# Optimization experiments

Measured on AMD Instinct MI355X. Metric: run time of the kernel, lower is better.

The kernel has to match this reference:

```python
import jax, jax.numpy as jnp
import numpy as np

B, N, IN, OUT, H = 8, 1024, 256, 256, 4
D = OUT // H  # head_dim = 64


def setup_inputs() -> dict:
    key = jax.random.key(0)
    k1, k2, k3, k4 = jax.random.split(key, 4)
    h = jax.random.normal(k1, (B, N, IN), dtype=jnp.float32)
    # torch Linear weight: [out, in], Wh = h @ W.T
    W = jax.random.normal(k2, (H * D, IN), dtype=jnp.float32) * (1.0 / np.sqrt(IN))
    # attention vector a: [n_heads, 2*head_dim] (xavier-uniform-ish scale)
    a = jax.random.normal(k3, (H, 2 * D), dtype=jnp.float32) * 0.1
    adj_mask = jax.random.bernoulli(k4, 0.1, (B, N, N))
    # ensure every row has at least one neighbor (self-loop) to avoid all -inf rows
    adj_mask = adj_mask | jnp.eye(N, dtype=bool)[None]
    return {"h": h, "W": W, "a": a, "adj_mask": adj_mask}


def reference(h, W, a, adj_mask):
    # Wh: [B, H, N, D]
    Wh = (h @ W.T).reshape(B, N, H, D).transpose(0, 2, 1, 3)
    # Split 'a' into src/dst halves: e_ij = leaky_relu(a_src.Wh_i + a_dst.Wh_j)
    # (mathematically identical to the original concat+einsum, without the N^2*2D tensor)
    src = jnp.einsum('bhnd,hd->bhn', Wh, a[:, :D])
    dst = jnp.einsum('bhnd,hd->bhn', Wh, a[:, D:])
    e = jax.nn.leaky_relu(src[:, :, :, None] + dst[:, :, None, :], negative_slope=0.2)
    e = jnp.where(adj_mask[:, None, :, :], e, -jnp.inf)
    att = jax.nn.softmax(e, axis=-1)
    att = jnp.where(jnp.isnan(att), 0.0, att)
    # dropout in eval mode -> identity
    h_prime = jnp.einsum('bhij,bhjd->bhid', att, Wh)
    # concat=True: [B, N, H*D]
    return h_prime.transpose(0, 2, 1, 3).reshape(B, N, H * D)
```

## Files before the change

### kernel.cpp

```cpp
#include <hip/hip_runtime.h>
#include <hip/hip_bf16.h>

#define B 8
#define N 1024
#define IN 256
#define H 4
#define D 64
#define O 256
#define BN (B*N)

typedef __attribute__((ext_vector_type(4))) float f32x4;
typedef __attribute__((ext_vector_type(8))) short short8;
typedef __attribute__((ext_vector_type(4))) short short4v;

__device__ __forceinline__ short f2bf(float f){
  __hip_bfloat16 b = __float2bfloat16(f);
  return __builtin_bit_cast(short, b);
}

#define PACK_BLOCKS 1024
#define CVT_BLOCKS  1056
#define H_ELEMS (BN*IN)
__global__ __launch_bounds__(256) void k_prep(const int* __restrict__ adj,
                                              unsigned* __restrict__ bits,
                                              const float* __restrict__ hmat,
                                              const float* __restrict__ Wmat,
                                              short* __restrict__ hbf,
                                              short* __restrict__ wbf){
  if(blockIdx.x < PACK_BLOCKS){
    int t = blockIdx.x * 256 + threadIdx.x;
    const int4* p = (const int4*)(adj + ((size_t)t << 5));
    unsigned word = 0;
    #pragma unroll
    for(int k = 0; k < 8; k++){
      int4 m = p[k];
      word |= (m.x != 0 ? 1u : 0u) << (k*4 + 0);
      word |= (m.y != 0 ? 1u : 0u) << (k*4 + 1);
      word |= (m.z != 0 ? 1u : 0u) << (k*4 + 2);
      word |= (m.w != 0 ? 1u : 0u) << (k*4 + 3);
    }
    bits[t] = word;
  } else {
    int idx = (blockIdx.x - PACK_BLOCKS) * 256 + threadIdx.x;
    int e = idx * 8;
    const float* srcp; short* dstp;
    if(e < H_ELEMS){ srcp = hmat + e; dstp = hbf + e; }
    else           { srcp = Wmat + (e - H_ELEMS); dstp = wbf + (e - H_ELEMS); }
    float4 a0 = *(const float4*)srcp;
    float4 a1 = *(const float4*)(srcp + 4);
    short8 pk;
    pk[0]=f2bf(a0.x); pk[1]=f2bf(a0.y); pk[2]=f2bf(a0.z); pk[3]=f2bf(a0.w);
    pk[4]=f2bf(a1.x); pk[5]=f2bf(a1.y); pk[6]=f2bf(a1.z); pk[7]=f2bf(a1.w);
    *(short8*)dstp = pk;
  }
}

__global__ __launch_bounds__(256) void k_wh(const short* __restrict__ hbf,
                                            const short* __restrict__ wbf,
                                            const float* __restrict__ avec,
                                            short* __restrict__ VT,
                                            float* __restrict__ src,
                                            float* __restrict__ dst){
  const int t = threadIdx.x;
  const int hh = t >> 6, lane = t & 63, quad = lane >> 4, l16 = lane & 15;
  const int mbase = blockIdx.x * 16;
  f32x4 acc[4];
  #pragma unroll
  for(int x=0;x<4;x++) acc[x] = (f32x4){0.f,0.f,0.f,0.f};
  const short* ap = hbf + (size_t)(mbase + l16) * IN + quad * 8;
  const short* bp0 = wbf + (size_t)(hh * 64 + l16) * IN + quad * 8;
  #pragma unroll
  for(int kk = 0; kk < 8; kk++){
    const int k0 = kk * 32;
    short8 A = *(const short8*)(ap + k0);
    #pragma unroll
    for(int dt=0; dt<4; dt++){
      short8 Bf = *(const short8*)(bp0 + (size_t)dt*16*IN + k0);
      acc[dt] = __builtin_amdgcn_mfma_f32_16x16x32_bf16(A, Bf, acc[dt], 0, 0, 0);
    }
  }
  const int bb = mbase >> 10;
  const int nb = (mbase & (N-1)) + quad * 4;
  const int bh = bb * H + hh;
  #pragma unroll
  for(int dt=0; dt<4; dt++){
    int d = dt*16 + l16;
    short4v pk;
    pk[0]=f2bf(acc[dt][0]); pk[1]=f2bf(acc[dt][1]);
    pk[2]=f2bf(acc[dt][2]); pk[3]=f2bf(acc[dt][3]);
    *(short4v*)(VT + (((size_t)bh * D + d) << 10) + nb) = pk;
  }
  float as[4], ad[4];
  #pragma unroll
  for(int dt=0; dt<4; dt++){
    as[dt] = avec[hh*(2*D) + dt*16 + l16];
    ad[dt] = avec[hh*(2*D) + D + dt*16 + l16];
  }
  #pragma unroll
  for(int r=0; r<4; r++){
    float s = 0.f, dd = 0.f;
    #pragma unroll
    for(int dt=0; dt<4; dt++){ s += acc[dt][r]*as[dt]; dd += acc[dt][r]*ad[dt]; }
    #pragma unroll
    for(int off=1; off<16; off<<=1){
      s  += __shfl_xor(s, off, 64);
      dd += __shfl_xor(dd, off, 64);
    }
    if(l16 == 0){
      int n = nb + r;
      src[(size_t)bh * N + n] = s;
      dst[(size_t)bh * N + n] = dd;
    }
  }
}

__global__ __launch_bounds__(256, 4) void k_attn(const short* __restrict__ VT,
                                              const float* __restrict__ src,
                                              const float* __restrict__ dst,
                                              const unsigned* __restrict__ bits,
                                              float* __restrict__ out){
  __shared__ float dsh[N];
  const int t = threadIdx.x;
  const int wave = t >> 6, lane = t & 63, quad = lane >> 4, l16 = lane & 15;
  const int b = blockIdx.z, hh = blockIdx.y;
  const int bh = b * H + hh;
  const int i0 = blockIdx.x * 64;
  #pragma unroll
  for(int j = t; j < N; j += 256) dsh[j] = dst[(size_t)bh * N + j];
  const int i = i0 + wave * 16 + l16;
  const float si = src[(size_t)bh * N + i];
  const int4* mp = (const int4*)(bits + ((size_t)b * N + i) * 32);
  int4 mv[8];
  #pragma unroll
  for(int k=0;k<8;k++) mv[k] = mp[k];
  const unsigned* mw = (const unsigned*)mv;
  const short* vrow = VT + (((size_t)bh * D) << 10) + quad * 8;
  short8 ones;
  #pragma unroll
  for(int k=0;k<8;k++) ones[k] = (short)0x3F80;
  f32x4 acc[4], accl;
  #pragma unroll
  for(int x=0;x<4;x++) acc[x] = (f32x4){0.f,0.f,0.f,0.f};
  accl = (f32x4){0.f,0.f,0.f,0.f};
  short8 buf[3][4];
  #pragma unroll
  for(int pre=0; pre<2; pre++)
    #pragma unroll
    for(int dt=0; dt<4; dt++)
      buf[pre][dt] = *(const short8*)(vrow + (((size_t)(dt*16 + l16)) << 10) + pre*32);
  __syncthreads();
  #pragma unroll
  for(int jt = 0; jt < 32; jt++){
    const int cur = jt % 3, nxt = (jt + 2) % 3;
    if(jt + 2 < 32){
      #pragma unroll
      for(int dt=0; dt<4; dt++)
        buf[nxt][dt] = *(const short8*)(vrow + (((size_t)(dt*16 + l16)) << 10) + (jt+2)*32);
    }
    const int j0 = jt * 32;
    const unsigned word = mw[jt];
    float4 d0 = *(const float4*)&dsh[j0 + quad*8];
    float4 d1 = *(const float4*)&dsh[j0 + quad*8 + 4];
    float dv[8] = {d0.x,d0.y,d0.z,d0.w,d1.x,d1.y,d1.z,d1.w};
    short8 P;
    #pragma unroll
    for(int jj=0; jj<8; jj++){
      float e = si + dv[jj];
      e = fmaxf(e, 0.2f * e);
      float p = ((word >> (quad*8 + jj)) & 1u) ? __expf(e) : 0.f;
      P[jj] = f2bf(p);
    }
    accl = __builtin_amdgcn_mfma_f32_16x16x32_bf16(P, ones, accl, 0, 0, 0);
    #pragma unroll
    for(int dt=0; dt<4; dt++)
      acc[dt] = __builtin_amdgcn_mfma_f32_16x16x32_bf16(P, buf[cur][dt], acc[dt], 0, 0, 0);
  }
  #pragma unroll
  for(int r=0; r<4; r++){
    float inv = 1.0f / accl[r];
    int ig = i0 + wave*16 + quad*4 + r;
    float* op = out + ((size_t)b * N + ig) * O + hh * D + l16;
    #pragma unroll
    for(int dt=0; dt<4; dt++) op[dt*16] = acc[dt][r] * inv;
  }
}

extern "C" void kernel_launch(void* const* d_in, const int* in_sizes, int n_in,
                              void* d_out, int out_size, void* d_ws, size_t ws_size,
                              hipStream_t stream) {
  const float* hmat = (const float*)d_in[0];
  const float* Wmat = (const float*)d_in[1];
  const float* avec = (const float*)d_in[2];
  const int* adj    = (const int*)d_in[3];
  float* out = (float*)d_out;
  char* ws = (char*)d_ws;
  short*    VT    = (short*)   (ws);
  short*    hbf   = (short*)   (ws + (size_t) 4*1024*1024);
  short*    wbf   = (short*)   (ws + (size_t) 8*1024*1024);
  unsigned* bits  = (unsigned*)(ws + (size_t) 9*1024*1024);
  float*    src   = (float*)   (ws + (size_t)10*1024*1024);
  float*    dst   = (float*)   (ws + (size_t)10*1024*1024 + 131072);
  k_prep<<<PACK_BLOCKS + CVT_BLOCKS, 256, 0, stream>>>(adj, bits, hmat, Wmat, hbf, wbf);
  k_wh<<<BN/16, 256, 0, stream>>>(hbf, wbf, avec, VT, src, dst);
  k_attn<<<dim3(16, H, B), 256, 0, stream>>>(VT, src, dst, bits, out);
}
```

Before: 130.5 us.

## Fuse bf16 conversion into Wh GEMM, merge prep kernels, restructure attention loop

Drops the separate fp32-to-bf16 conversion pass. The Wh GEMM now reads fp32 h and W and converts them in registers, and it shares one launch with the adjacency bit-packing, which removes a kernel launch and an intermediate round trip through memory. src/dst are pre-scaled by log2(e) so the attention loop can use exp2 instead of exp. That loop switches to a double-buffered, manually grouped schedule that streams mask words and dst values instead of preloading all of them, and the occupancy hint drops from 4 to 2. The cost is that W is re-read and reconverted by every GEMM block, and occupancy may fall.

```diff
diff --git a/kernel.cpp b/kernel.cpp
--- a/kernel.cpp
+++ b/kernel.cpp
@@ -8,6 +8,7 @@
 #define D 64
 #define O 256
 #define BN (B*N)
+#define LOG2E 1.4426950408889634f
 
 typedef __attribute__((ext_vector_type(4))) float f32x4;
 typedef __attribute__((ext_vector_type(8))) short short8;
@@ -18,17 +19,26 @@
   return __builtin_bit_cast(short, b);
 }
 
+__device__ __forceinline__ short8 pack8(float4 a0, float4 a1){
+  short8 pk;
+  pk[0]=f2bf(a0.x); pk[1]=f2bf(a0.y); pk[2]=f2bf(a0.z); pk[3]=f2bf(a0.w);
+  pk[4]=f2bf(a1.x); pk[5]=f2bf(a1.y); pk[6]=f2bf(a1.z); pk[7]=f2bf(a1.w);
+  return pk;
+}
+
+#define WH_BLOCKS  (BN/16)
 #define PACK_BLOCKS 1024
-#define CVT_BLOCKS  1056
-#define H_ELEMS (BN*IN)
-__global__ __launch_bounds__(256) void k_prep(const int* __restrict__ adj,
-                                              unsigned* __restrict__ bits,
-                                              const float* __restrict__ hmat,
-                                              const float* __restrict__ Wmat,
-                                              short* __restrict__ hbf,
-                                              short* __restrict__ wbf){
-  if(blockIdx.x < PACK_BLOCKS){
-    int t = blockIdx.x * 256 + threadIdx.x;
+
+__global__ __launch_bounds__(256) void k1(const int* __restrict__ adj,
+                                          unsigned* __restrict__ bits,
+                                          const float* __restrict__ hmat,
+                                          const float* __restrict__ Wmat,
+                                          const float* __restrict__ avec,
+                                          short* __restrict__ VT,
+                                          float* __restrict__ src,
+                                          float* __restrict__ dst){
+  if(blockIdx.x >= WH_BLOCKS){
+    int t = (blockIdx.x - WH_BLOCKS) * 256 + threadIdx.x;
     const int4* p = (const int4*)(adj + ((size_t)t << 5));
     unsigned word = 0;
     #pragma unroll
@@ -40,42 +50,28 @@
       word |= (m.w != 0 ? 1u : 0u) << (k*4 + 3);
     }
     bits[t] = word;
-  } else {
-    int idx = (blockIdx.x - PACK_BLOCKS) * 256 + threadIdx.x;
-    int e = idx * 8;
-    const float* srcp; short* dstp;
-    if(e < H_ELEMS){ srcp = hmat + e; dstp = hbf + e; }
-    else           { srcp = Wmat + (e - H_ELEMS); dstp = wbf + (e - H_ELEMS); }
-    float4 a0 = *(const float4*)srcp;
-    float4 a1 = *(const float4*)(srcp + 4);
-    short8 pk;
-    pk[0]=f2bf(a0.x); pk[1]=f2bf(a0.y); pk[2]=f2bf(a0.z); pk[3]=f2bf(a0.w);
-    pk[4]=f2bf(a1.x); pk[5]=f2bf(a1.y); pk[6]=f2bf(a1.z); pk[7]=f2bf(a1.w);
-    *(short8*)dstp = pk;
-  }
-}
-
-__global__ __launch_bounds__(256) void k_wh(const short* __restrict__ hbf,
-                                            const short* __restrict__ wbf,
-                                            const float* __restrict__ avec,
-                                            short* __restrict__ VT,
-                                            float* __restrict__ src,
-                                            float* __restrict__ dst){
+    return;
+  }
   const int t = threadIdx.x;
   const int hh = t >> 6, lane = t & 63, quad = lane >> 4, l16 = lane & 15;
   const int mbase = blockIdx.x * 16;
   f32x4 acc[4];
   #pragma unroll
   for(int x=0;x<4;x++) acc[x] = (f32x4){0.f,0.f,0.f,0.f};
-  const short* ap = hbf + (size_t)(mbase + l16) * IN + quad * 8;
-  const short* bp0 = wbf + (size_t)(hh * 64 + l16) * IN + quad * 8;
+  const float* ap  = hmat + (size_t)(mbase + l16) * IN + quad * 8;
+  const float* bp0 = Wmat + (size_t)(hh * 64 + l16) * IN + quad * 8;
   #pragma unroll
   for(int kk = 0; kk < 8; kk++){
     const int k0 = kk * 32;
-    short8 A = *(const short8*)(ap + k0);
+    float4 a0 = *(const float4*)(ap + k0);
+    float4 a1 = *(const float4*)(ap + k0 + 4);
+    short8 A = pack8(a0, a1);
     #pragma unroll
     for(int dt=0; dt<4; dt++){
-      short8 Bf = *(const short8*)(bp0 + (size_t)dt*16*IN + k0);
+      const float* bp = bp0 + (size_t)dt*16*IN + k0;
+      float4 b0 = *(const float4*)bp;
+      float4 b1 = *(const float4*)(bp + 4);
+      short8 Bf = pack8(b0, b1);
       acc[dt] = __builtin_amdgcn_mfma_f32_16x16x32_bf16(A, Bf, acc[dt], 0, 0, 0);
     }
   }
@@ -108,17 +104,17 @@
     }
     if(l16 == 0){
       int n = nb + r;
-      src[(size_t)bh * N + n] = s;
-      dst[(size_t)bh * N + n] = dd;
-    }
-  }
-}
-
-__global__ __launch_bounds__(256, 4) void k_attn(const short* __restrict__ VT,
-                                              const float* __restrict__ src,
-                                              const float* __restrict__ dst,
-                                              const unsigned* __restrict__ bits,
-                                              float* __restrict__ out){
+      src[(size_t)bh * N + n] = s  * LOG2E;
+      dst[(size_t)bh * N + n] = dd * LOG2E;
+    }
+  }
+}
+
+__global__ __launch_bounds__(256, 2) void k_attn(const short* __restrict__ VT,
+                                                 const float* __restrict__ src,
+                                                 const float* __restrict__ dst,
+                                                 const unsigned* __restrict__ bits,
+                                                 float* __restrict__ out){
   __shared__ float dsh[N];
   const int t = threadIdx.x;
   const int wave = t >> 6, lane = t & 63, quad = lane >> 4, l16 = lane & 15;
@@ -130,10 +126,8 @@
   const int i = i0 + wave * 16 + l16;
   const float si = src[(size_t)bh * N + i];
   const int4* mp = (const int4*)(bits + ((size_t)b * N + i) * 32);
-  int4 mv[8];
-  #pragma unroll
-  for(int k=0;k<8;k++) mv[k] = mp[k];
-  const unsigned* mw = (const unsigned*)mv;
+  int4 mcur = mp[0];
+  int4 mnext = mp[1];
   const short* vrow = VT + (((size_t)bh * D) << 10) + quad * 8;
   short8 ones;
   #pragma unroll
@@ -142,39 +136,52 @@
   #pragma unroll
   for(int x=0;x<4;x++) acc[x] = (f32x4){0.f,0.f,0.f,0.f};
   accl = (f32x4){0.f,0.f,0.f,0.f};
-  short8 buf[3][4];
-  #pragma unroll
-  for(int pre=0; pre<2; pre++)
-    #pragma unroll
-    for(int dt=0; dt<4; dt++)
-      buf[pre][dt] = *(const short8*)(vrow + (((size_t)(dt*16 + l16)) << 10) + pre*32);
+  short8 bufA[4], bufB[4];
+  #pragma unroll
+  for(int dt=0; dt<4; dt++)
+    bufA[dt] = *(const short8*)(vrow + (((size_t)(dt*16 + l16)) << 10));
   __syncthreads();
-  #pragma unroll
-  for(int jt = 0; jt < 32; jt++){
-    const int cur = jt % 3, nxt = (jt + 2) % 3;
-    if(jt + 2 < 32){
-      #pragma unroll
-      for(int dt=0; dt<4; dt++)
-        buf[nxt][dt] = *(const short8*)(vrow + (((size_t)(dt*16 + l16)) << 10) + (jt+2)*32);
-    }
-    const int j0 = jt * 32;
-    const unsigned word = mw[jt];
-    float4 d0 = *(const float4*)&dsh[j0 + quad*8];
-    float4 d1 = *(const float4*)&dsh[j0 + quad*8 + 4];
-    float dv[8] = {d0.x,d0.y,d0.z,d0.w,d1.x,d1.y,d1.z,d1.w};
-    short8 P;
-    #pragma unroll
-    for(int jj=0; jj<8; jj++){
-      float e = si + dv[jj];
-      e = fmaxf(e, 0.2f * e);
-      float p = ((word >> (quad*8 + jj)) & 1u) ? __expf(e) : 0.f;
-      P[jj] = f2bf(p);
-    }
-    accl = __builtin_amdgcn_mfma_f32_16x16x32_bf16(P, ones, accl, 0, 0, 0);
-    #pragma unroll
-    for(int dt=0; dt<4; dt++)
-      acc[dt] = __builtin_amdgcn_mfma_f32_16x16x32_bf16(P, buf[cur][dt], acc[dt], 0, 0, 0);
-  }
+  float4 dA0 = *(const float4*)&dsh[quad*8];
+  float4 dA1 = *(const float4*)&dsh[quad*8 + 4];
+  float4 dB0, dB1;
+
+#define STEP(JT, BC, BNX, DC0, DC1, DN0, DN1, WORD) do {                        \
+    if((JT) < 31){                                                              \
+      _Pragma("unroll")                                                         \
+      for(int dt=0; dt<4; dt++)                                                 \
+        BNX[dt] = *(const short8*)(vrow + (((size_t)(dt*16 + l16)) << 10)       \
+                                   + ((JT)+1)*32);                              \
+      DN0 = *(const float4*)&dsh[((JT)+1)*32 + quad*8];                         \
+      DN1 = *(const float4*)&dsh[((JT)+1)*32 + quad*8 + 4];                     \
+    }                                                                           \
+    const unsigned wsh = ((unsigned)(WORD)) >> (quad*8);                        \
+    float dvv[8] = {DC0.x,DC0.y,DC0.z,DC0.w,DC1.x,DC1.y,DC1.z,DC1.w};           \
+    short8 P;                                                                   \
+    _Pragma("unroll")                                                           \
+    for(int jj=0; jj<8; jj++){                                                  \
+      float e = si + dvv[jj];                                                   \
+      float l = fmaxf(e, 0.2f * e);              \
+      float p = ((wsh >> jj) & 1u) ? __builtin_exp2f(l) : 0.f;                  \
+      P[jj] = f2bf(p);                                                          \
+    }                                                                           \
+    accl = __builtin_amdgcn_mfma_f32_16x16x32_bf16(P, ones, accl, 0, 0, 0);     \
+    _Pragma("unroll")                                                           \
+    for(int dt=0; dt<4; dt++)                                                   \
+      acc[dt] = __builtin_amdgcn_mfma_f32_16x16x32_bf16(P, BC[dt], acc[dt],     \
+                                                        0, 0, 0);               \
+  } while(0)
+
+  for(int g = 0; g < 8; ++g){
+    const int jt0 = g * 4;
+    STEP(jt0+0, bufA, bufB, dA0, dA1, dB0, dB1, mcur.x);
+    STEP(jt0+1, bufB, bufA, dB0, dB1, dA0, dA1, mcur.y);
+    STEP(jt0+2, bufA, bufB, dA0, dA1, dB0, dB1, mcur.z);
+    STEP(jt0+3, bufB, bufA, dB0, dB1, dA0, dA1, mcur.w);
+    mcur = mnext;
+    if(g < 6) mnext = mp[g + 2];
+  }
+#undef STEP
+
   #pragma unroll
   for(int r=0; r<4; r++){
     float inv = 1.0f / accl[r];
@@ -194,13 +201,10 @@
   const int* adj    = (const int*)d_in[3];
   float* out = (float*)d_out;
   char* ws = (char*)d_ws;
-  short*    VT    = (short*)   (ws);
-  short*    hbf   = (short*)   (ws + (size_t) 4*1024*1024);
-  short*    wbf   = (short*)   (ws + (size_t) 8*1024*1024);
-  unsigned* bits  = (unsigned*)(ws + (size_t) 9*1024*1024);
-  float*    src   = (float*)   (ws + (size_t)10*1024*1024);
-  float*    dst   = (float*)   (ws + (size_t)10*1024*1024 + 131072);
-  k_prep<<<PACK_BLOCKS + CVT_BLOCKS, 256, 0, stream>>>(adj, bits, hmat, Wmat, hbf, wbf);
-  k_wh<<<BN/16, 256, 0, stream>>>(hbf, wbf, avec, VT, src, dst);
+  short*    VT   = (short*)   (ws);
+  unsigned* bits = (unsigned*)(ws + (size_t)4*1024*1024);
+  float*    src  = (float*)   (ws + (size_t)5*1024*1024);
+  float*    dst  = (float*)   (ws + (size_t)5*1024*1024 + 131072);
+  k1<<<WH_BLOCKS + PACK_BLOCKS, 256, 0, stream>>>(adj, bits, hmat, Wmat, avec, VT, src, dst);
   k_attn<<<dim3(16, H, B), 256, 0, stream>>>(VT, src, dst, bits, out);
 }
```

Result: slower. 137.6 us (+5.5%).
